# Kernel tuning notes

Hardware: AMD Instinct MI355X
Metric: run time of the kernel (lower is better)

The kernel has to match this reference:

```python
import jax, jax.numpy as jnp
import numpy as np

B, C, H, W = 4, 96, 64, 64
CS = 8                      # chunk size
DN = 2 * C                  # d_inner (expand=2)
N = 16                      # d_state
K = 4                       # scan directions
DT_R = (C + 15) // 16       # dt_rank = ceil(d_model/16)
EPS = 1e-5


def _ln(x, g, b):
    m = x.mean(-1, keepdims=True)
    v = ((x - m) ** 2).mean(-1, keepdims=True)
    return (x - m) / jnp.sqrt(v + EPS) * g + b


def _selective_scan(xs, delta, A, Bs, Cs, D):
    # xs, delta: (Bc, K, Dn, L); Bs, Cs: (Bc, K, N, L); A: (K, Dn, N); D: (K, Dn)
    Bc, Kk, Dn, L = xs.shape
    uT = xs.transpose(3, 0, 1, 2)       # (L, Bc, K, Dn)
    dT = delta.transpose(3, 0, 1, 2)
    BT = Bs.transpose(3, 0, 1, 2)       # (L, Bc, K, N)
    CT = Cs.transpose(3, 0, 1, 2)

    def step(h, inp):
        u_l, d_l, B_l, C_l = inp
        dA = jnp.exp(d_l[..., None] * A)                       # (Bc,K,Dn,N)
        h = h * dA + (d_l * u_l)[..., None] * B_l[:, :, None, :]
        y = jnp.einsum('bkdn,bkn->bkd', h, C_l)
        return h, y

    h0 = jnp.zeros((Bc, Kk, Dn, A.shape[-1]), xs.dtype)
    _, ys = jax.lax.scan(step, h0, (uT, dT, BT, CT))           # ys: (L,Bc,K,Dn)
    ys = ys.transpose(1, 2, 3, 0)                              # (Bc,K,Dn,L)
    return ys + D[None, :, :, None] * xs


def _ss2d(xh, in_proj_w, conv_w, conv_b, x_proj_w, dt_w, dt_b,
          A_logs, Ds, outnorm_g, outnorm_b, out_proj_w):
    # xh: (Bc, Hc, Wc, C)
    Bc, Hc, Wc, _ = xh.shape
    L = Hc * Wc
    xz = xh @ in_proj_w                                        # (Bc,Hc,Wc,2*Dn)
    xc, z = jnp.split(xz, 2, axis=-1)
    xc = xc.transpose(0, 3, 1, 2)                              # (Bc,Dn,Hc,Wc)
    xc = jax.lax.conv_general_dilated(xc, conv_w, (1, 1), ((1, 1), (1, 1)),
                                      feature_group_count=DN)
    xc = jax.nn.silu(xc + conv_b[None, :, None, None])
    x0 = xc.reshape(Bc, DN, L)                                 # HW order
    x1 = xc.transpose(0, 1, 3, 2).reshape(Bc, DN, L)           # WH order
    xs = jnp.stack([x0, x1, x0[:, :, ::-1], x1[:, :, ::-1]], axis=1)  # (Bc,4,Dn,L)
    x_dbl = jnp.einsum('bkdl,kcd->bkcl', xs, x_proj_w)         # (Bc,4,DT_R+2N,L)
    dts = x_dbl[:, :, :DT_R]
    Bs = x_dbl[:, :, DT_R:DT_R + N]
    Cs = x_dbl[:, :, DT_R + N:]
    dts = jnp.einsum('bkrl,kdr->bkdl', dts, dt_w)
    delta = jax.nn.softplus(dts + dt_b[None, :, :, None])      # (Bc,4,Dn,L)
    A = -jnp.exp(A_logs).reshape(K, DN, N)
    ys = _selective_scan(xs, delta, A, Bs, Cs, Ds.reshape(K, DN))
    y0 = ys[:, 0]
    y1 = ys[:, 1].reshape(Bc, DN, Wc, Hc).transpose(0, 1, 3, 2).reshape(Bc, DN, L)
    y2 = ys[:, 2, :, ::-1]
    y3 = ys[:, 3, :, ::-1].reshape(Bc, DN, Wc, Hc).transpose(0, 1, 3, 2).reshape(Bc, DN, L)
    y = (y0 + y1 + y2 + y3).transpose(0, 2, 1)                 # (Bc,L,Dn)
    y = _ln(y, outnorm_g, outnorm_b).reshape(Bc, Hc, Wc, DN)
    y = y * jax.nn.silu(z)
    return y @ out_proj_w                                      # (Bc,Hc,Wc,C)


def reference(x, gamma, beta, alpha, ln1_g, ln1_b, in_proj_w, conv_w, conv_b,
              x_proj_w, dt_w, dt_b, A_logs, Ds, outnorm_g, outnorm_b, out_proj_w):
    Bb, Cc, Hh, Ww = x.shape
    # StateNorm: per (b, c) over spatial dims, unbiased=False
    mean = x.mean(axis=(2, 3), keepdims=True)
    var = ((x - mean) ** 2).mean(axis=(2, 3), keepdims=True)
    x_norm = (x - mean) / jnp.sqrt(var + EPS)
    x_norm = gamma[None, :, None, None] * x_norm + beta[None, :, None, None]
    x_act = jax.nn.silu(x_norm)                 # act_quant with bits=32 is identity
    hn, wn = Hh // CS, Ww // CS
    # chunk: b c (hn cs)(wn cs) -> (b hn wn) c cs cs
    xc = x_act.reshape(Bb, Cc, hn, CS, wn, CS).transpose(0, 2, 4, 1, 3, 5)
    xc = xc.reshape(Bb * hn * wn, Cc, CS, CS)
    # VSSBlock: h + SS2D(LN(h)) in BHWC (drop_path = identity at inference)
    h = xc.transpose(0, 2, 3, 1)                # (Bc, cs, cs, C)
    h = h + _ss2d(_ln(h, ln1_g, ln1_b), in_proj_w, conv_w, conv_b, x_proj_w,
                  dt_w, dt_b, A_logs, Ds, outnorm_g, outnorm_b, out_proj_w)
    xv = h.transpose(0, 3, 1, 2)                # back to BCHW
    # unchunk
    xv = xv.reshape(Bb, hn, wn, Cc, CS, CS).transpose(0, 3, 1, 4, 2, 5)
    xv = xv.reshape(Bb, Cc, Hh, Ww)
    return x + alpha * xv


def setup_inputs() -> dict:
    key = jax.random.key(0)
    ks = jax.random.split(key, 12)
    s = 0.02
    inp = {
        'x': jax.random.normal(ks[0], (B, C, H, W), jnp.float32),
        'gamma': jnp.ones((C,), jnp.float32),
        'beta': jnp.zeros((C,), jnp.float32),
        'alpha': jnp.float32(0.5),
        'ln1_g': jnp.ones((C,), jnp.float32),
        'ln1_b': jnp.zeros((C,), jnp.float32),
        'in_proj_w': jax.random.normal(ks[1], (C, 2 * DN), jnp.float32) / np.sqrt(C),
        'conv_w': jax.random.normal(ks[2], (DN, 1, 3, 3), jnp.float32) / 3.0,
        'conv_b': jnp.zeros((DN,), jnp.float32),
        'x_proj_w': jax.random.normal(ks[3], (K, DT_R + 2 * N, DN), jnp.float32) / np.sqrt(DN),
        'dt_w': jax.random.normal(ks[4], (K, DN, DT_R), jnp.float32) * (DT_R ** -0.5),
        'dt_b': jnp.full((K, DN), -4.6, jnp.float32) + s * jax.random.normal(ks[5], (K, DN), jnp.float32),
        'A_logs': jnp.log(jnp.broadcast_to(jnp.arange(1, N + 1, dtype=jnp.float32), (K * DN, N))).copy(),
        'Ds': jnp.ones((K * DN,), jnp.float32),
        'outnorm_g': jnp.ones((DN,), jnp.float32),
        'outnorm_b': jnp.zeros((DN,), jnp.float32),
        'out_proj_w': jax.random.normal(ks[6], (DN, C), jnp.float32) / np.sqrt(DN),
    }
    return inp
```

## Files before the change

kernel.cpp:

```cpp
#include <hip/hip_runtime.h>
#include <math.h>

__device__ __forceinline__ float siluf_(float x) {
    return x / (1.f + __expf(-x));
}

__device__ __forceinline__ int sperm(int k, int l) {
    int t = (k & 1) ? (((l & 7) << 3) | (l >> 3)) : l;
    return (k & 2) ? (63 - t) : t;
}

__device__ __forceinline__ unsigned int f2bf(float f) {
    unsigned int u = __float_as_uint(f);
    return (u + 0x7FFFu + ((u >> 16) & 1u)) >> 16;
}
__device__ __forceinline__ float bf2f(unsigned int h) {
    return __uint_as_float(h << 16);
}
__device__ __forceinline__ unsigned int packbf(float lo, float hi) {
    return f2bf(lo) | (f2bf(hi) << 16);
}

__global__ void k1a_stats(const float* __restrict__ x, float* __restrict__ stats) {
    int bc = blockIdx.x;
    const float* xp = x + (size_t)bc * 4096;
    float s = 0.f, sq = 0.f;
    for (int i = threadIdx.x; i < 4096; i += 256) {
        float v = xp[i]; s += v; sq += v * v;
    }
    __shared__ float rs[256], rq[256];
    rs[threadIdx.x] = s; rq[threadIdx.x] = sq;
    __syncthreads();
    for (int off = 128; off > 0; off >>= 1) {
        if (threadIdx.x < off) {
            rs[threadIdx.x] += rs[threadIdx.x + off];
            rq[threadIdx.x] += rq[threadIdx.x + off];
        }
        __syncthreads();
    }
    if (threadIdx.x == 0) {
        float m = rs[0] * (1.f / 4096.f);
        float v = rq[0] * (1.f / 4096.f) - m * m;
        stats[bc] = m;
        stats[384 + bc] = rsqrtf(v + 1e-5f);
    }
}

__global__ __launch_bounds__(256) void kA(
        const float* __restrict__ x, const float* __restrict__ stats,
        const float* __restrict__ gamma, const float* __restrict__ beta,
        const float* __restrict__ ln1_g, const float* __restrict__ ln1_b,
        const float* __restrict__ Win,
        float* __restrict__ xcg_all,
        unsigned int* __restrict__ zg_b) {
    int blk = blockIdx.x;
    int xcd = blk & 7, j = blk >> 3;
    int chunk = xcd * 32 + (j >> 2), cg = j & 3;
    int b = chunk >> 6, chh = (chunk >> 3) & 7, chw = chunk & 7;
    __shared__ float hs[64 * 97];
    int t = threadIdx.x;
    for (int i = t; i < 6144; i += 256) {
        int c = i >> 6, pos = i & 63;
        int bc = b * 96 + c;
        int hh = chh * 8 + (pos >> 3), ww = chw * 8 + (pos & 7);
        float v = x[(((size_t)bc) * 64 + hh) * 64 + ww];
        float xn = (v - stats[bc]) * stats[384 + bc] * gamma[c] + beta[c];
        hs[pos * 97 + c] = siluf_(xn);
    }
    __syncthreads();
    {
        int p = t >> 2, o = t & 3;
        float s = 0.f, sq = 0.f;
        #pragma unroll
        for (int jj = 0; jj < 24; jj++) { float v = hs[p * 97 + o + 4 * jj]; s += v; sq += v * v; }
        s += __shfl_xor(s, 1); sq += __shfl_xor(sq, 1);
        s += __shfl_xor(s, 2); sq += __shfl_xor(sq, 2);
        float m = s * (1.f / 96.f);
        float rinv = rsqrtf(sq * (1.f / 96.f) - m * m + 1e-5f);
        #pragma unroll
        for (int jj = 0; jj < 24; jj++) {
            int c = o + 4 * jj;
            hs[p * 97 + c] = (hs[p * 97 + c] - m) * rinv * ln1_g[c] + ln1_b[c];
        }
    }
    __syncthreads();
    int p = t & 63;
    int wv = __builtin_amdgcn_readfirstlane(t >> 6);
    int jbase = cg * 96 + wv * 24;
    float acc[24];
    #pragma unroll
    for (int i = 0; i < 24; i++) acc[i] = 0.f;
    for (int c = 0; c < 96; c++) {
        float u = hs[p * 97 + c];
        const float* w = Win + c * 384 + jbase;
        #pragma unroll
        for (int i = 0; i < 24; i++) acc[i] = fmaf(u, w[i], acc[i]);
    }
    if (jbase < 192) {
        float* o_ = xcg_all + (size_t)chunk * 12288 + jbase * 64 + p;
        #pragma unroll
        for (int i = 0; i < 24; i++) o_[i * 64] = acc[i];
    } else {
        int i2base = (jbase - 192) >> 1;
        unsigned int* o_ = zg_b + (size_t)chunk * 6144 + i2base * 64 + p;
        #pragma unroll
        for (int i = 0; i < 12; i++) o_[i * 64] = packbf(acc[2 * i], acc[2 * i + 1]);
    }
}

__global__ __launch_bounds__(256) void kB(
        const float* __restrict__ xcg_all, const float* __restrict__ conv_w,
        const float* __restrict__ conv_b, float* __restrict__ x0T_all) {
    int blk = blockIdx.x;
    int xcd = blk & 7, j = blk >> 3;
    int chunk = xcd * 32 + (j >> 2), dg = j & 3;
    int dbase = dg * 48;
    __shared__ float tile[48 * 65];
    int t = threadIdx.x;
    const float* in = xcg_all + (size_t)chunk * 12288 + dbase * 64;
    for (int i = t; i < 3072; i += 256) tile[(i >> 6) * 65 + (i & 63)] = in[i];
    __syncthreads();
    float* o = x0T_all + (size_t)chunk * 12288;
    for (int s = 0; s < 12; s++) {
        int idx = s * 256 + t;
        int l = idx / 48, dl = idx - l * 48;
        int r = l >> 3, cc = l & 7;
        int d = dbase + dl;
        float acc = conv_b[d];
        #pragma unroll
        for (int dh = 0; dh < 3; dh++) {
            int rr = r + dh - 1;
            if (rr < 0 || rr > 7) continue;
            #pragma unroll
            for (int dw = 0; dw < 3; dw++) {
                int cw = cc + dw - 1;
                if (cw < 0 || cw > 7) continue;
                acc = fmaf(tile[dl * 65 + rr * 8 + cw], conv_w[d * 9 + dh * 3 + dw], acc);
            }
        }
        o[l * 192 + d] = siluf_(acc);
    }
}

__global__ __launch_bounds__(192, 3) void kD(
        const float* __restrict__ x0T_all, const float* __restrict__ xpw,
        const float* __restrict__ dtw, const float* __restrict__ dtb,
        const float* __restrict__ A_logs, const float* __restrict__ Ds,
        unsigned int* __restrict__ yk01,
        unsigned int* __restrict__ yk23) {
    int blk = blockIdx.x;
    int xcd = blk & 7, j = blk >> 3;
    int chunk = xcd * 32 + (j >> 2);
    int k = j & 3;
    __shared__ float pT[64 * 40];
    int t = threadIdx.x;
    const float* xbase = x0T_all + (size_t)chunk * 12288;

    {
        int l = t & 63;
        int wv3 = __builtin_amdgcn_readfirstlane(t >> 6);
        int cbase = wv3 * 13;
        float acc[13];
        #pragma unroll
        for (int i = 0; i < 13; i++) acc[i] = 0.f;
        const float* xl = xbase + l * 192;
        const float* wb = xpw + (size_t)k * 38 * 192;
        for (int dd = 0; dd < 192; dd += 4) {
            float4 u4 = *(const float4*)(xl + dd);
            #pragma unroll
            for (int ci = 0; ci < 13; ci++) {
                int c = cbase + ci;
                if (c < 38) {
                    float4 w4 = *(const float4*)(wb + c * 192 + dd);
                    acc[ci] = fmaf(u4.x, w4.x, acc[ci]);
                    acc[ci] = fmaf(u4.y, w4.y, acc[ci]);
                    acc[ci] = fmaf(u4.z, w4.z, acc[ci]);
                    acc[ci] = fmaf(u4.w, w4.w, acc[ci]);
                }
            }
        }
        #pragma unroll
        for (int ci = 0; ci < 13; ci++) {
            int c = cbase + ci;
            if (c < 38) {
                int slot = c + (c >= 6 ? 2 : 0);
                pT[l * 40 + slot] = acc[ci];
            }
        }
    }
    __syncthreads();

    {
        int d = t;
        int gd = k * 192 + d;
        float w6[6];
        #pragma unroll
        for (int r = 0; r < 6; r++) w6[r] = dtw[gd * 6 + r];
        float bias = dtb[gd];
        float Dd = Ds[gd];
        float a[16];
        #pragma unroll
        for (int n = 0; n < 16; n++) a[n] = -__expf(A_logs[gd * 16 + n]);
        bool pw = true;
        #pragma unroll
        for (int n = 1; n < 16; n++)
            pw = pw && (fabsf(a[n] - (float)(n + 1) * a[0]) <= 1e-4f * fabsf(a[n]) + 1e-6f);
        float hst[16];
        #pragma unroll
        for (int n = 0; n < 16; n++) hst[n] = 0.f;
        unsigned int* yb = (k < 2 ? yk01 : yk23) + (size_t)(k & 1) * 1572864
                           + (size_t)chunk * 6144;

        if (__all(pw)) {
            float a0 = a[0];
            int sl = sperm(k, 0);
            const float4* r4 = (const float4*)(pT + sl * 40);
            float4 rA = r4[0], rB = r4[1];
            float4 b0 = r4[2], b1 = r4[3], b2 = r4[4], b3 = r4[5];
            float4 c0 = r4[6], c1 = r4[7], c2 = r4[8], c3 = r4[9];
            float u = xbase[sl * 192 + d];
            #pragma unroll 2
            for (int l = 0; l < 64; l++) {
                int sl_n = sperm(k, (l + 1) & 63);
                const float4* n4 = (const float4*)(pT + sl_n * 40);
                float4 nA = n4[0], nB = n4[1];
                float4 nb0 = n4[2], nb1 = n4[3], nb2 = n4[4], nb3 = n4[5];
                float4 nc0 = n4[6], nc1 = n4[7], nc2 = n4[8], nc3 = n4[9];
                float u_n = xbase[sl_n * 192 + d];
                float dp = bias;
                dp = fmaf(rA.x, w6[0], dp); dp = fmaf(rA.y, w6[1], dp);
                dp = fmaf(rA.z, w6[2], dp); dp = fmaf(rA.w, w6[3], dp);
                dp = fmaf(rB.x, w6[4], dp); dp = fmaf(rB.y, w6[5], dp);
                float delta = (dp > 20.f) ? dp : __logf(1.f + __expf(dp));
                float du = delta * u;
                float e1 = __expf(delta * a0);
                float p[16];
                p[0] = e1;
                p[1] = e1 * e1;
                p[2] = p[1] * e1;   p[3] = p[1] * p[1];
                p[4] = p[3] * e1;   p[5] = p[3] * p[1];
                p[6] = p[3] * p[2]; p[7] = p[3] * p[3];
                p[8] = p[7] * e1;   p[9] = p[7] * p[1];
                p[10] = p[7] * p[2]; p[11] = p[7] * p[3];
                p[12] = p[7] * p[4]; p[13] = p[7] * p[5];
                p[14] = p[7] * p[6]; p[15] = p[7] * p[7];
                float y0 = 0.f, y1 = 0.f, y2 = 0.f, y3 = 0.f;
                hst[0]  = fmaf(hst[0],  p[0],  du * b0.x); y0 = fmaf(hst[0],  c0.x, y0);
                hst[1]  = fmaf(hst[1],  p[1],  du * b0.y); y1 = fmaf(hst[1],  c0.y, y1);
                hst[2]  = fmaf(hst[2],  p[2],  du * b0.z); y2 = fmaf(hst[2],  c0.z, y2);
                hst[3]  = fmaf(hst[3],  p[3],  du * b0.w); y3 = fmaf(hst[3],  c0.w, y3);
                hst[4]  = fmaf(hst[4],  p[4],  du * b1.x); y0 = fmaf(hst[4],  c1.x, y0);
                hst[5]  = fmaf(hst[5],  p[5],  du * b1.y); y1 = fmaf(hst[5],  c1.y, y1);
                hst[6]  = fmaf(hst[6],  p[6],  du * b1.z); y2 = fmaf(hst[6],  c1.z, y2);
                hst[7]  = fmaf(hst[7],  p[7],  du * b1.w); y3 = fmaf(hst[7],  c1.w, y3);
                hst[8]  = fmaf(hst[8],  p[8],  du * b2.x); y0 = fmaf(hst[8],  c2.x, y0);
                hst[9]  = fmaf(hst[9],  p[9],  du * b2.y); y1 = fmaf(hst[9],  c2.y, y1);
                hst[10] = fmaf(hst[10], p[10], du * b2.z); y2 = fmaf(hst[10], c2.z, y2);
                hst[11] = fmaf(hst[11], p[11], du * b2.w); y3 = fmaf(hst[11], c2.w, y3);
                hst[12] = fmaf(hst[12], p[12], du * b3.x); y0 = fmaf(hst[12], c3.x, y0);
                hst[13] = fmaf(hst[13], p[13], du * b3.y); y1 = fmaf(hst[13], c3.y, y1);
                hst[14] = fmaf(hst[14], p[14], du * b3.z); y2 = fmaf(hst[14], c3.z, y2);
                hst[15] = fmaf(hst[15], p[15], du * b3.w); y3 = fmaf(hst[15], c3.w, y3);
                float yv = (y0 + y1) + (y2 + y3) + Dd * u;
                float yo = __shfl_xor(yv, 1);
                unsigned int wpack = packbf(yv, yo);
                if ((d & 1) == 0) yb[sl * 96 + (d >> 1)] = wpack;
                rA = nA; rB = nB;
                b0 = nb0; b1 = nb1; b2 = nb2; b3 = nb3;
                c0 = nc0; c1 = nc1; c2 = nc2; c3 = nc3;
                u = u_n; sl = sl_n;
            }
        } else {
            for (int l = 0; l < 64; l++) {
                int sl = sperm(k, l);
                float u = xbase[sl * 192 + d];
                const float* row = pT + sl * 40;
                float dp = bias;
                #pragma unroll
                for (int r = 0; r < 6; r++) dp = fmaf(row[r], w6[r], dp);
                float delta = (dp > 20.f) ? dp : __logf(1.f + __expf(dp));
                float du = delta * u;
                float y = 0.f;
                #pragma unroll
                for (int n = 0; n < 16; n++) {
                    float e = __expf(delta * a[n]);
                    hst[n] = fmaf(hst[n], e, du * row[8 + n]);
                    y = fmaf(hst[n], row[24 + n], y);
                }
                float yv = y + Dd * u;
                float yo = __shfl_xor(yv, 1);
                unsigned int wpack = packbf(yv, yo);
                if ((d & 1) == 0) yb[sl * 96 + (d >> 1)] = wpack;
            }
        }
    }
}

__global__ __launch_bounds__(256) void kE(
        const unsigned int* __restrict__ yk01, const unsigned int* __restrict__ yk23,
        const unsigned int* __restrict__ zg_b,
        const float* __restrict__ og, const float* __restrict__ ob,
        float* __restrict__ g_all) {
    int blk = blockIdx.x;
    int xcd = blk & 7, j = blk >> 3;
    int chunk = xcd * 32 + (j >> 1), half = j & 1;
    int t = threadIdx.x;
    int p = half * 32 + (t >> 3), o = t & 7;
    int par = o & 1;
    size_t rb = (size_t)chunk * 6144 + p * 96;
    const unsigned int* r0 = yk01 + rb;
    const unsigned int* r1 = yk01 + 1572864 + rb;
    const unsigned int* r2 = yk23 + rb;
    const unsigned int* r3 = yk23 + 1572864 + rb;
    float ys[24];
    float s = 0.f, sq = 0.f;
    #pragma unroll
    for (int jj = 0; jj < 24; jj++) {
        int i = o + 8 * jj;
        int wi = i >> 1;
        int sh = par ? 16 : 0;
        float v = bf2f((r0[wi] >> sh) & 0xFFFFu) + bf2f((r1[wi] >> sh) & 0xFFFFu)
                + bf2f((r2[wi] >> sh) & 0xFFFFu) + bf2f((r3[wi] >> sh) & 0xFFFFu);
        ys[jj] = v; s += v; sq += v * v;
    }
    s += __shfl_xor(s, 1); sq += __shfl_xor(sq, 1);
    s += __shfl_xor(s, 2); sq += __shfl_xor(sq, 2);
    s += __shfl_xor(s, 4); sq += __shfl_xor(sq, 4);
    float m = s * (1.f / 192.f);
    float rinv = rsqrtf(sq * (1.f / 192.f) - m * m + 1e-5f);
    const unsigned int* z = zg_b + (size_t)chunk * 6144;
    float* g = g_all + (size_t)chunk * 12288;
    #pragma unroll
    for (int jj = 0; jj < 24; jj++) {
        int i = o + 8 * jj;
        float ln = (ys[jj] - m) * rinv * og[i] + ob[i];
        unsigned int zw = z[(i >> 1) * 64 + p];
        float zv = bf2f(par ? (zw >> 16) : (zw & 0xFFFFu));
        g[i * 64 + p] = ln * siluf_(zv);
    }
}

__global__ __launch_bounds__(256) void kF(
        const float* __restrict__ g_all, const float* __restrict__ Wout,
        const float* __restrict__ x, const float* __restrict__ stats,
        const float* __restrict__ gamma, const float* __restrict__ beta,
        const float* __restrict__ alpha, float* __restrict__ out) {
    int blk = blockIdx.x;
    int xcd = blk & 7, j = blk >> 3;
    int chunk = xcd * 32 + (j >> 2), cgf = j & 3;
    int b = chunk >> 6, chh = (chunk >> 3) & 7, chw = chunk & 7;
    int t = threadIdx.x;
    int p = t & 63;
    int wv = __builtin_amdgcn_readfirstlane(t >> 6);
    int cbase = cgf * 24 + wv * 6;
    float acc[6];
    #pragma unroll
    for (int i = 0; i < 6; i++) acc[i] = 0.f;
    const float* g = g_all + (size_t)chunk * 12288;
    for (int dd = 0; dd < 192; dd++) {
        float u = g[dd * 64 + p];
        const float* w = Wout + dd * 96 + cbase;
        #pragma unroll
        for (int i = 0; i < 6; i++) acc[i] = fmaf(u, w[i], acc[i]);
    }
    float al = alpha[0];
    int hh = chh * 8 + (p >> 3), ww = chw * 8 + (p & 7);
    #pragma unroll
    for (int i = 0; i < 6; i++) {
        int c = cbase + i;
        int bc = b * 96 + c;
        size_t gi = (((size_t)bc) * 64 + hh) * 64 + ww;
        float xv = x[gi];
        float xn = (xv - stats[bc]) * stats[384 + bc] * gamma[c] + beta[c];
        out[gi] = xv + al * (siluf_(xn) + acc[i]);
    }
}

extern "C" void kernel_launch(void* const* d_in, const int* in_sizes, int n_in,
                              void* d_out, int out_size, void* d_ws, size_t ws_size,
                              hipStream_t stream) {
    const float* x        = (const float*)d_in[0];
    const float* gamma    = (const float*)d_in[1];
    const float* beta     = (const float*)d_in[2];
    const float* alpha    = (const float*)d_in[3];
    const float* ln1_g    = (const float*)d_in[4];
    const float* ln1_b    = (const float*)d_in[5];
    const float* in_proj  = (const float*)d_in[6];
    const float* conv_w   = (const float*)d_in[7];
    const float* conv_b   = (const float*)d_in[8];
    const float* x_proj   = (const float*)d_in[9];
    const float* dt_w     = (const float*)d_in[10];
    const float* dt_b     = (const float*)d_in[11];
    const float* A_logs   = (const float*)d_in[12];
    const float* Ds       = (const float*)d_in[13];
    const float* onorm_g  = (const float*)d_in[14];
    const float* onorm_b  = (const float*)d_in[15];
    const float* out_proj = (const float*)d_in[16];
    float* out = (float*)d_out;

    float* ws    = (float*)d_ws;
    float* stats = ws;
    float* xcg   = ws + 768;
    float* x0T   = xcg + 3145728;
    unsigned int* zg_b = (unsigned int*)(x0T + 3145728);
    unsigned int* yk23 = zg_b + 1572864;
    unsigned int* yk01 = (unsigned int*)xcg;
    float* gbuf  = x0T;

    hipLaunchKernelGGL(k1a_stats, dim3(384), dim3(256), 0, stream, x, stats);
    hipLaunchKernelGGL(kA, dim3(1024), dim3(256), 0, stream,
                       x, stats, gamma, beta, ln1_g, ln1_b, in_proj, xcg, zg_b);
    hipLaunchKernelGGL(kB, dim3(1024), dim3(256), 0, stream,
                       xcg, conv_w, conv_b, x0T);
    hipLaunchKernelGGL(kD, dim3(1024), dim3(192), 0, stream,
                       x0T, x_proj, dt_w, dt_b, A_logs, Ds, yk01, yk23);
    hipLaunchKernelGGL(kE, dim3(512), dim3(256), 0, stream,
                       yk01, yk23, zg_b, onorm_g, onorm_b, gbuf);
    hipLaunchKernelGGL(kF, dim3(1024), dim3(256), 0, stream,
                       gbuf, out_proj, x, stats, gamma, beta, alpha, out);
}
```

Measured before the change: 208.6 us.

## Split scan state across two threads per channel in selective-scan kernel

The scan kernel now uses 384 threads per block. Each channel's 16 state elements are split into two halves of 8, one per thread, and the partial outputs are combined with a lane shuffle. The x_proj stage is spread over six waves with 7 outputs each, and the u values are batched into groups of 8 loads per step. The aim is to cut per-thread register pressure and serial latency so more waves can hide the exp and FMA dependency chains. The cost is an extra exp per step, duplicated delta computation in both halves, and more shuffles.

```diff
diff --git a/kernel.cpp b/kernel.cpp
--- a/kernel.cpp
+++ b/kernel.cpp
@@ -142,7 +142,7 @@
     }
 }
 
-__global__ __launch_bounds__(192, 3) void kD(
+__global__ __launch_bounds__(384, 6) void kD(
         const float* __restrict__ x0T_all, const float* __restrict__ xpw,
         const float* __restrict__ dtw, const float* __restrict__ dtb,
         const float* __restrict__ A_logs, const float* __restrict__ Ds,
@@ -158,17 +158,17 @@
 
     {
         int l = t & 63;
-        int wv3 = __builtin_amdgcn_readfirstlane(t >> 6);
-        int cbase = wv3 * 13;
-        float acc[13];
-        #pragma unroll
-        for (int i = 0; i < 13; i++) acc[i] = 0.f;
+        int wv6 = __builtin_amdgcn_readfirstlane(t >> 6);
+        int cbase = wv6 * 7;
+        float acc[7];
+        #pragma unroll
+        for (int i = 0; i < 7; i++) acc[i] = 0.f;
         const float* xl = xbase + l * 192;
         const float* wb = xpw + (size_t)k * 38 * 192;
         for (int dd = 0; dd < 192; dd += 4) {
             float4 u4 = *(const float4*)(xl + dd);
             #pragma unroll
-            for (int ci = 0; ci < 13; ci++) {
+            for (int ci = 0; ci < 7; ci++) {
                 int c = cbase + ci;
                 if (c < 38) {
                     float4 w4 = *(const float4*)(wb + c * 192 + dd);
@@ -180,7 +180,7 @@
             }
         }
         #pragma unroll
-        for (int ci = 0; ci < 13; ci++) {
+        for (int ci = 0; ci < 7; ci++) {
             int c = cbase + ci;
             if (c < 38) {
                 int slot = c + (c >= 6 ? 2 : 0);
@@ -191,84 +191,69 @@
     __syncthreads();
 
     {
-        int d = t;
+        int d = t >> 1, h = t & 1;
         int gd = k * 192 + d;
         float w6[6];
         #pragma unroll
         for (int r = 0; r < 6; r++) w6[r] = dtw[gd * 6 + r];
         float bias = dtb[gd];
-        float Dd = Ds[gd];
-        float a[16];
-        #pragma unroll
-        for (int n = 0; n < 16; n++) a[n] = -__expf(A_logs[gd * 16 + n]);
+        float Dd_eff = h ? 0.f : Ds[gd];
+        float a0 = -__expf(A_logs[gd * 16]);
+        float a8[8];
+        #pragma unroll
+        for (int n = 0; n < 8; n++) a8[n] = -__expf(A_logs[gd * 16 + 8 * h + n]);
         bool pw = true;
         #pragma unroll
-        for (int n = 1; n < 16; n++)
-            pw = pw && (fabsf(a[n] - (float)(n + 1) * a[0]) <= 1e-4f * fabsf(a[n]) + 1e-6f);
-        float hst[16];
-        #pragma unroll
-        for (int n = 0; n < 16; n++) hst[n] = 0.f;
+        for (int n = 0; n < 8; n++) {
+            float tgt = (float)(8 * h + n + 1) * a0;
+            pw = pw && (fabsf(a8[n] - tgt) <= 1e-4f * fabsf(tgt) + 1e-6f);
+        }
+        float c0 = a0 * (float)(8 * h + 1);
+        float hst[8];
+        #pragma unroll
+        for (int n = 0; n < 8; n++) hst[n] = 0.f;
         unsigned int* yb = (k < 2 ? yk01 : yk23) + (size_t)(k & 1) * 1572864
                            + (size_t)chunk * 6144;
+        int h4 = 2 * h;
 
         if (__all(pw)) {
-            float a0 = a[0];
-            int sl = sperm(k, 0);
-            const float4* r4 = (const float4*)(pT + sl * 40);
-            float4 rA = r4[0], rB = r4[1];
-            float4 b0 = r4[2], b1 = r4[3], b2 = r4[4], b3 = r4[5];
-            float4 c0 = r4[6], c1 = r4[7], c2 = r4[8], c3 = r4[9];
-            float u = xbase[sl * 192 + d];
-            #pragma unroll 2
-            for (int l = 0; l < 64; l++) {
-                int sl_n = sperm(k, (l + 1) & 63);
-                const float4* n4 = (const float4*)(pT + sl_n * 40);
-                float4 nA = n4[0], nB = n4[1];
-                float4 nb0 = n4[2], nb1 = n4[3], nb2 = n4[4], nb3 = n4[5];
-                float4 nc0 = n4[6], nc1 = n4[7], nc2 = n4[8], nc3 = n4[9];
-                float u_n = xbase[sl_n * 192 + d];
-                float dp = bias;
-                dp = fmaf(rA.x, w6[0], dp); dp = fmaf(rA.y, w6[1], dp);
-                dp = fmaf(rA.z, w6[2], dp); dp = fmaf(rA.w, w6[3], dp);
-                dp = fmaf(rB.x, w6[4], dp); dp = fmaf(rB.y, w6[5], dp);
-                float delta = (dp > 20.f) ? dp : __logf(1.f + __expf(dp));
-                float du = delta * u;
-                float e1 = __expf(delta * a0);
-                float p[16];
-                p[0] = e1;
-                p[1] = e1 * e1;
-                p[2] = p[1] * e1;   p[3] = p[1] * p[1];
-                p[4] = p[3] * e1;   p[5] = p[3] * p[1];
-                p[6] = p[3] * p[2]; p[7] = p[3] * p[3];
-                p[8] = p[7] * e1;   p[9] = p[7] * p[1];
-                p[10] = p[7] * p[2]; p[11] = p[7] * p[3];
-                p[12] = p[7] * p[4]; p[13] = p[7] * p[5];
-                p[14] = p[7] * p[6]; p[15] = p[7] * p[7];
-                float y0 = 0.f, y1 = 0.f, y2 = 0.f, y3 = 0.f;
-                hst[0]  = fmaf(hst[0],  p[0],  du * b0.x); y0 = fmaf(hst[0],  c0.x, y0);
-                hst[1]  = fmaf(hst[1],  p[1],  du * b0.y); y1 = fmaf(hst[1],  c0.y, y1);
-                hst[2]  = fmaf(hst[2],  p[2],  du * b0.z); y2 = fmaf(hst[2],  c0.z, y2);
-                hst[3]  = fmaf(hst[3],  p[3],  du * b0.w); y3 = fmaf(hst[3],  c0.w, y3);
-                hst[4]  = fmaf(hst[4],  p[4],  du * b1.x); y0 = fmaf(hst[4],  c1.x, y0);
-                hst[5]  = fmaf(hst[5],  p[5],  du * b1.y); y1 = fmaf(hst[5],  c1.y, y1);
-                hst[6]  = fmaf(hst[6],  p[6],  du * b1.z); y2 = fmaf(hst[6],  c1.z, y2);
-                hst[7]  = fmaf(hst[7],  p[7],  du * b1.w); y3 = fmaf(hst[7],  c1.w, y3);
-                hst[8]  = fmaf(hst[8],  p[8],  du * b2.x); y0 = fmaf(hst[8],  c2.x, y0);
-                hst[9]  = fmaf(hst[9],  p[9],  du * b2.y); y1 = fmaf(hst[9],  c2.y, y1);
-                hst[10] = fmaf(hst[10], p[10], du * b2.z); y2 = fmaf(hst[10], c2.z, y2);
-                hst[11] = fmaf(hst[11], p[11], du * b2.w); y3 = fmaf(hst[11], c2.w, y3);
-                hst[12] = fmaf(hst[12], p[12], du * b3.x); y0 = fmaf(hst[12], c3.x, y0);
-                hst[13] = fmaf(hst[13], p[13], du * b3.y); y1 = fmaf(hst[13], c3.y, y1);
-                hst[14] = fmaf(hst[14], p[14], du * b3.z); y2 = fmaf(hst[14], c3.z, y2);
-                hst[15] = fmaf(hst[15], p[15], du * b3.w); y3 = fmaf(hst[15], c3.w, y3);
-                float yv = (y0 + y1) + (y2 + y3) + Dd * u;
-                float yo = __shfl_xor(yv, 1);
-                unsigned int wpack = packbf(yv, yo);
-                if ((d & 1) == 0) yb[sl * 96 + (d >> 1)] = wpack;
-                rA = nA; rB = nB;
-                b0 = nb0; b1 = nb1; b2 = nb2; b3 = nb3;
-                c0 = nc0; c1 = nc1; c2 = nc2; c3 = nc3;
-                u = u_n; sl = sl_n;
+            for (int g8 = 0; g8 < 8; ++g8) {
+                float u8[8];
+                #pragma unroll
+                for (int i = 0; i < 8; i++)
+                    u8[i] = xbase[sperm(k, g8 * 8 + i) * 192 + d];
+                #pragma unroll
+                for (int i = 0; i < 8; i++) {
+                    int sl = sperm(k, g8 * 8 + i);
+                    const float4* r4 = (const float4*)(pT + sl * 40);
+                    float4 rA = r4[0], rB = r4[1];
+                    float dp = bias;
+                    dp = fmaf(rA.x, w6[0], dp); dp = fmaf(rA.y, w6[1], dp);
+                    dp = fmaf(rA.z, w6[2], dp); dp = fmaf(rA.w, w6[3], dp);
+                    dp = fmaf(rB.x, w6[4], dp); dp = fmaf(rB.y, w6[5], dp);
+                    float delta = (dp > 20.f) ? dp : __logf(1.f + __expf(dp));
+                    float du = delta * u8[i];
+                    float e1 = __expf(delta * a0);
+                    float eb = __expf(delta * c0);
+                    float e2 = e1 * e1, e4 = e2 * e2;
+                    float p0 = eb,      p1 = eb * e1, p2 = eb * e2, p3 = p1 * e2;
+                    float p4 = p0 * e4, p5 = p1 * e4, p6 = p2 * e4, p7 = p3 * e4;
+                    float4 bq0 = r4[2 + h4], bq1 = r4[3 + h4];
+                    float4 cq0 = r4[6 + h4], cq1 = r4[7 + h4];
+                    float y0, y1;
+                    hst[0] = fmaf(hst[0], p0, du * bq0.x); y0 = hst[0] * cq0.x;
+                    hst[1] = fmaf(hst[1], p1, du * bq0.y); y1 = hst[1] * cq0.y;
+                    hst[2] = fmaf(hst[2], p2, du * bq0.z); y0 = fmaf(hst[2], cq0.z, y0);
+                    hst[3] = fmaf(hst[3], p3, du * bq0.w); y1 = fmaf(hst[3], cq0.w, y1);
+                    hst[4] = fmaf(hst[4], p4, du * bq1.x); y0 = fmaf(hst[4], cq1.x, y0);
+                    hst[5] = fmaf(hst[5], p5, du * bq1.y); y1 = fmaf(hst[5], cq1.y, y1);
+                    hst[6] = fmaf(hst[6], p6, du * bq1.z); y0 = fmaf(hst[6], cq1.z, y0);
+                    hst[7] = fmaf(hst[7], p7, du * bq1.w); y1 = fmaf(hst[7], cq1.w, y1);
+                    float yp = fmaf(Dd_eff, u8[i], y0 + y1);
+                    float yfull = yp + __shfl_xor(yp, 1);
+                    float yo2 = __shfl_xor(yfull, 2);
+                    if ((t & 3) == 0) yb[sl * 96 + (d >> 1)] = packbf(yfull, yo2);
+                }
             }
         } else {
             for (int l = 0; l < 64; l++) {
@@ -280,17 +265,17 @@
                 for (int r = 0; r < 6; r++) dp = fmaf(row[r], w6[r], dp);
                 float delta = (dp > 20.f) ? dp : __logf(1.f + __expf(dp));
                 float du = delta * u;
-                float y = 0.f;
+                float yp = 0.f;
                 #pragma unroll
-                for (int n = 0; n < 16; n++) {
-                    float e = __expf(delta * a[n]);
-                    hst[n] = fmaf(hst[n], e, du * row[8 + n]);
-                    y = fmaf(hst[n], row[24 + n], y);
+                for (int n = 0; n < 8; n++) {
+                    float e = __expf(delta * a8[n]);
+                    hst[n] = fmaf(hst[n], e, du * row[8 + 8 * h + n]);
+                    yp = fmaf(hst[n], row[24 + 8 * h + n], yp);
                 }
-                float yv = y + Dd * u;
-                float yo = __shfl_xor(yv, 1);
-                unsigned int wpack = packbf(yv, yo);
-                if ((d & 1) == 0) yb[sl * 96 + (d >> 1)] = wpack;
+                yp = fmaf(Dd_eff, u, yp);
+                float yfull = yp + __shfl_xor(yp, 1);
+                float yo2 = __shfl_xor(yfull, 2);
+                if ((t & 3) == 0) yb[sl * 96 + (d >> 1)] = packbf(yfull, yo2);
             }
         }
     }
@@ -412,7 +397,7 @@
                        x, stats, gamma, beta, ln1_g, ln1_b, in_proj, xcg, zg_b);
     hipLaunchKernelGGL(kB, dim3(1024), dim3(256), 0, stream,
                        xcg, conv_w, conv_b, x0T);
-    hipLaunchKernelGGL(kD, dim3(1024), dim3(192), 0, stream,
+    hipLaunchKernelGGL(kD, dim3(1024), dim3(384), 0, stream,
                        x0T, x_proj, dt_w, dt_b, A_logs, Ds, yk01, yk23);
     hipLaunchKernelGGL(kE, dim3(512), dim3(256), 0, stream,
                        yk01, yk23, zg_b, onorm_g, onorm_b, gbuf);
```

Result: faster. 203.6 us (-2.4%).
